# Performance work log

Hardware: AMD Instinct MI355X
Metric: run time of the kernel (lower is better)

Reference implementation:

```python
import jax, jax.numpy as jnp
import numpy as np

B, L, S, D, H = 2, 384, 384, 512, 256
BASE_TEMP = 10.0
LN_EPS = 1e-5


def setup_inputs() -> dict:
    key = jax.random.key(0)
    ks = jax.random.split(key, 12)
    return {
        "q": jax.random.normal(ks[0], (B, L, D), jnp.float32),
        "k": jax.random.normal(ks[1], (B, S, D), jnp.float32),
        "q_global": jax.random.normal(ks[2], (B, D), jnp.float32),
        "k_global": jax.random.normal(ks[3], (B, D), jnp.float32),
        "W1": jax.random.normal(ks[4], (4 * D, H), jnp.float32) * (1.0 / np.sqrt(4 * D)),
        "b1": jnp.zeros((H,), jnp.float32),
        "gamma": jnp.ones((H,), jnp.float32),
        "beta": jnp.zeros((H,), jnp.float32),
        "W2": jax.random.normal(ks[5], (H, 1), jnp.float32) * (1.0 / np.sqrt(H)),
        "b2": jnp.zeros((1,), jnp.float32),
        "gumbel_u": jax.random.uniform(ks[6], (B, L, S, 2), jnp.float32),
    }


def reference(q, k, q_global, k_global, W1, b1, gamma, beta, W2, b2, gumbel_u):
    d = q.shape[-1]
    # Decompose Linear(4D,H) on the [q, k, q_global, k_global] concat into
    # four per-tensor projections; sum broadcasts to the pairwise grid.
    Wq, Wk, Wqg, Wkg = jnp.split(W1, 4, axis=0)  # each [D,H]
    hq = q @ Wq + (q_global @ Wqg)[:, None, :]   # [B,L,H]
    hk = k @ Wk + (k_global @ Wkg)[:, None, :]   # [B,S,H]
    h = hq[:, :, None, :] + hk[:, None, :, :] + b1  # [B,L,S,H]
    h = jax.nn.gelu(h, approximate=False)
    mu = jnp.mean(h, axis=-1, keepdims=True)
    var = jnp.mean(jnp.square(h - mu), axis=-1, keepdims=True)
    h = (h - mu) * jax.lax.rsqrt(var + LN_EPS) * gamma + beta
    thresholds = (h @ W2)[..., 0] + b2[0]  # [B,L,S]
    sim = jnp.einsum("bld,bsd->bls", q, k) / jnp.sqrt(jnp.float32(d))
    logits = (sim - thresholds) / BASE_TEMP
    binary_logits = jnp.stack([-logits, logits], axis=-1)  # [B,L,S,2]
    u = jnp.clip(gumbel_u, 1e-6, 1.0 - 1e-6)
    g = -jnp.log(-jnp.log(u))
    soft = jax.nn.softmax(binary_logits + g, axis=-1)  # tau=1.0
    hard = jax.nn.one_hot(jnp.argmax(soft, axis=-1), 2, dtype=soft.dtype)
    y = hard + soft - jax.lax.stop_gradient(soft)  # straight-through
    return y[..., 1][:, None, :, :]  # [B,1,L,S]
```

## Files before the change

kernel.cpp:

```cpp
#include <hip/hip_runtime.h>
#include <hip/hip_bf16.h>
#include <math.h>

#define Bb 2
#define Lq 384
#define Sk 384
#define Dd 512
#define Hh 256

#define LIST_CAP 65536

#define HQD_OFF  0
#define HKD_OFF  (HQD_OFF + Bb*Lq*Hh*8)
#define GQD_OFF  (HKD_OFF + Bb*Sk*Hh*8)
#define GKD_OFF  (GQD_OFF + Bb*Hh*8)
#define HQ_OFF   (GKD_OFF + Bb*Hh*8)
#define HK_OFF   (HQ_OFF + Bb*Lq*Hh*4)
#define SIM0_OFF (HK_OFF + Bb*Sk*Hh*4)
#define SIM1_OFF (SIM0_OFF + Bb*Lq*Sk*4)
#define SCAL_OFF (SIM1_OFF + Bb*Lq*Sk*4)
#define GW_OFF   (SCAL_OFF + 64)
#define CNT_OFF  (GW_OFF + 1024)
#define LIST_OFF (CNT_OFF + 64)

__global__ __launch_bounds__(256) void smalls_kernel(
    const float* __restrict__ qg, const float* __restrict__ kg,
    const float* __restrict__ W1,
    const float* __restrict__ gam, const float* __restrict__ bet,
    const float* __restrict__ W2, const float* __restrict__ b2,
    double* __restrict__ gq_d, double* __restrict__ gk_d,
    float* __restrict__ gw_out, float* __restrict__ scal)
{
    __shared__ double red[64][5];
    __shared__ float2 red2[256];
    int bx  = blockIdx.x;
    int tid = threadIdx.x;
    if (bx < 16) {
        int isK = bx & 1;
        int b   = (bx >> 1) & 1;
        int hc  = bx >> 2;
        int hl  = tid >> 2;
        int dp  = tid & 3;
        int h   = hc * 64 + hl;
        const float* gv = (isK ? kg : qg) + b * Dd;
        const float* wp = W1 + (isK ? 3 : 2) * Dd * Hh + h;
        int d0 = dp * 128;
        double a0 = 0, a1 = 0, a2 = 0, a3 = 0;
        for (int i = 0; i < 128; i += 4) {
            int d = d0 + i;
            a0 = fma((double)gv[d + 0], (double)wp[(d + 0) * Hh], a0);
            a1 = fma((double)gv[d + 1], (double)wp[(d + 1) * Hh], a1);
            a2 = fma((double)gv[d + 2], (double)wp[(d + 2) * Hh], a2);
            a3 = fma((double)gv[d + 3], (double)wp[(d + 3) * Hh], a3);
        }
        red[hl][dp] = ((a0 + a1) + (a2 + a3));
        __syncthreads();
        if (dp == 0) {
            double s = (red[hl][0] + red[hl][1]) + (red[hl][2] + red[hl][3]);
            (isK ? gk_d : gq_d)[b * Hh + h] = s;
        }
    } else {
        float w2v = W2[tid];
        float gwv = gam[tid] * w2v;
        gw_out[tid] = gwv;
        red2[tid] = make_float2(gwv, bet[tid] * w2v);
        __syncthreads();
        for (int o = 128; o > 0; o >>= 1) {
            if (tid < o) {
                red2[tid].x += red2[tid + o].x;
                red2[tid].y += red2[tid + o].y;
            }
            __syncthreads();
        }
        if (tid == 0) {
            scal[0] = red2[0].x;
            scal[1] = red2[0].y + b2[0];
        }
    }
}

__global__ __launch_bounds__(512) void projd_kernel(
    const float* __restrict__ q, const float* __restrict__ k,
    const float* __restrict__ W1, const float* __restrict__ b1,
    const double* __restrict__ gq_d, const double* __restrict__ gk_d,
    double* __restrict__ hq_d, double* __restrict__ hk_d,
    float* __restrict__ hq, float* __restrict__ hk)
{
    __shared__ __align__(16) float smem[8 * 512];
    float  (*tile)[512] = (float (*)[512])smem;
    double (*pbuf)[256] = (double (*)[256])smem;
    int tid = threadIdx.x;
    int h   = tid & 255;
    int dh  = tid >> 8;
    int bx = blockIdx.x;
    bool isQ = bx < 96;
    int bb = isQ ? bx : bx - 96;
    int b  = bb / 48;
    int rg = bb % 48;
    const float*  src = isQ ? q : k;
    const double* gl  = isQ ? gq_d : gk_d;
    int woff = isQ ? 0 : Dd * Hh;
    double* dstd = isQ ? hq_d : hk_d;
    float*  dstf = isQ ? hq : hk;

    int base = (b * Lq + rg * 8) * Dd;
    for (int i = tid; i < 1024; i += 512)
        *reinterpret_cast<float4*>(&smem[i * 4]) =
            *reinterpret_cast<const float4*>(src + base + i * 4);
    __syncthreads();

    const float* wp = W1 + woff + (dh * 256) * Hh + h;
    int dbase = dh * 256;
    double acc[8];
#pragma unroll
    for (int r = 0; r < 8; ++r) acc[r] = 0.0;
#pragma unroll 2
    for (int d4 = 0; d4 < 256; d4 += 4) {
        double w0 = (double)wp[(d4 + 0) * Hh];
        double w1 = (double)wp[(d4 + 1) * Hh];
        double w2 = (double)wp[(d4 + 2) * Hh];
        double w3 = (double)wp[(d4 + 3) * Hh];
#pragma unroll
        for (int r = 0; r < 8; ++r) {
            float4 tv = *reinterpret_cast<const float4*>(&tile[r][dbase + d4]);
            acc[r] = fma((double)tv.x, w0, acc[r]);
            acc[r] = fma((double)tv.y, w1, acc[r]);
            acc[r] = fma((double)tv.z, w2, acc[r]);
            acc[r] = fma((double)tv.w, w3, acc[r]);
        }
    }
    __syncthreads();
    if (dh == 1) {
#pragma unroll
        for (int r = 0; r < 8; ++r) pbuf[r][h] = acc[r];
    }
    __syncthreads();
    if (dh == 0) {
        double gd  = gl[b * Hh + h];
        double b1d = isQ ? (double)b1[h] : 0.0;
        int ob = (b * Lq + rg * 8) * Hh + h;
#pragma unroll
        for (int r = 0; r < 8; ++r) {
            double tot = (acc[r] + pbuf[r][h]) + gd;
            dstd[ob + r * Hh] = tot;
            dstf[ob + r * Hh] = (float)(tot + b1d);
        }
    }
}

__global__ __launch_bounds__(256) void sim_kernel(
    const float* __restrict__ q, const float* __restrict__ k,
    float* __restrict__ sim01)
{
    __shared__ __align__(16) float qs[32][132];
    __shared__ __align__(16) float ks[32][132];
    int tid = threadIdx.x;
    int bx = blockIdx.x;
    int kc = (bx >= Bb * 144) ? 1 : 0;
    int r  = bx - kc * Bb * 144;
    int b  = r / 144;  r %= 144;
    int lt = r / 12, st = r % 12;
    int tl = tid >> 4, ts = tid & 15;
    const float* qb = q + (b * Lq + lt * 32) * Dd;
    const float* kb = k + (b * Sk + st * 32) * Dd;
    float a00 = 0.f, a01 = 0.f, a10 = 0.f, a11 = 0.f;
    for (int c = kc * 256; c < kc * 256 + 256; c += 128) {
        __syncthreads();
        for (int i = tid; i < 1024; i += 256) {
            int row = i >> 5;
            int c4  = (i & 31) << 2;
            *reinterpret_cast<float4*>(&qs[row][c4]) =
                *reinterpret_cast<const float4*>(qb + row * Dd + c + c4);
            *reinterpret_cast<float4*>(&ks[row][c4]) =
                *reinterpret_cast<const float4*>(kb + row * Dd + c + c4);
        }
        __syncthreads();
#pragma unroll 2
        for (int dd = 0; dd < 128; dd += 4) {
            float4 q0 = *reinterpret_cast<const float4*>(&qs[tl][dd]);
            float4 q1 = *reinterpret_cast<const float4*>(&qs[tl + 16][dd]);
            float4 k0 = *reinterpret_cast<const float4*>(&ks[ts][dd]);
            float4 k1 = *reinterpret_cast<const float4*>(&ks[ts + 16][dd]);
            a00 = fmaf(q0.x, k0.x, a00); a00 = fmaf(q0.y, k0.y, a00);
            a00 = fmaf(q0.z, k0.z, a00); a00 = fmaf(q0.w, k0.w, a00);
            a01 = fmaf(q0.x, k1.x, a01); a01 = fmaf(q0.y, k1.y, a01);
            a01 = fmaf(q0.z, k1.z, a01); a01 = fmaf(q0.w, k1.w, a01);
            a10 = fmaf(q1.x, k0.x, a10); a10 = fmaf(q1.y, k0.y, a10);
            a10 = fmaf(q1.z, k0.z, a10); a10 = fmaf(q1.w, k0.w, a10);
            a11 = fmaf(q1.x, k1.x, a11); a11 = fmaf(q1.y, k1.y, a11);
            a11 = fmaf(q1.z, k1.z, a11); a11 = fmaf(q1.w, k1.w, a11);
        }
    }
    const float sc = 0.04419417382415922f;
    float* dst = sim01 + kc * (Bb * Lq * Sk);
    int l0 = lt * 32 + tl, s0 = st * 32 + ts;
    dst[(b * Lq + l0)      * Sk + s0]      = a00 * sc;
    dst[(b * Lq + l0)      * Sk + s0 + 16] = a01 * sc;
    dst[(b * Lq + l0 + 16) * Sk + s0]      = a10 * sc;
    dst[(b * Lq + l0 + 16) * Sk + s0 + 16] = a11 * sc;
}

__device__ __forceinline__ void gelu2(float2 hqv, float2 hkv, float2 gwv,
                                      float2& s1, float2& s2, float2& sw)
{
    const float P2   = 0.23164189f;
    const float A1f = 0.254829592f, A2f = -0.284496736f, A3f = 1.421413741f,
                A4f = -1.453152027f, A5f = 1.061405429f;
    const float NL2EH = -0.72134752044448170f;

    float xa = hqv.x + hkv.x,        xb = hqv.y + hkv.y;
    float axa = fabsf(xa),           axb = fabsf(xb);
    float dda = fmaf(P2, axa, 1.0f), ddb = fmaf(P2, axb, 1.0f);
    float ta = __builtin_amdgcn_rcpf(dda), tb = __builtin_amdgcn_rcpf(ddb);
    float x2a = xa * xa,             x2b = xb * xb;
    float exa = __builtin_amdgcn_exp2f(x2a * NL2EH);
    float exb = __builtin_amdgcn_exp2f(x2b * NL2EH);
    float sa = fmaf(A5f, ta, A4f),   sb = fmaf(A5f, tb, A4f);
    sa = fmaf(sa, ta, A3f);          sb = fmaf(sb, tb, A3f);
    sa = fmaf(sa, ta, A2f);          sb = fmaf(sb, tb, A2f);
    sa = fmaf(sa, ta, A1f);          sb = fmaf(sb, tb, A1f);
    sa = sa * ta;                    sb = sb * tb;
    float Ea = fmaf(-sa, exa, 1.0f), Eb = fmaf(-sb, exb, 1.0f);
    float ya = fmaf(axa, Ea, xa),    yb = fmaf(axb, Eb, xb);
    s1.x += ya;                      s1.y += yb;
    s2.x = fmaf(ya, ya, s2.x);       s2.y = fmaf(yb, yb, s2.y);
    sw.x = fmaf(ya, gwv.x, sw.x);    sw.y = fmaf(yb, gwv.y, sw.y);
}

__global__ __launch_bounds__(256) void main_kernel(
    const float* __restrict__ hq, const float* __restrict__ hk,
    const float* __restrict__ sim0, const float* __restrict__ sim1,
    const float* __restrict__ gw_in, const float* __restrict__ scal,
    const float* __restrict__ gu, float* __restrict__ out,
    int* __restrict__ cnt, int* __restrict__ list)
{
    __shared__ __align__(16) float hq_t[16][260];
    __shared__ __align__(16) float hk_t[16][260];
    __shared__ __align__(16) float gw_s[256];
    int tid = threadIdx.x;
    int bx = blockIdx.x;
    int b  = bx / (24 * 24);
    int r  = bx % (24 * 24);
    int lt = r / 24, st = r % 24;

    const float* hqb = hq + (b * Lq + lt * 16) * Hh;
    const float* hkb = hk + (b * Sk + st * 16) * Hh;
#pragma unroll
    for (int i = 0; i < 4; ++i) {
        int idx4 = i * 256 + tid;
        int row  = idx4 >> 6;
        int col4 = (idx4 & 63) << 2;
        *reinterpret_cast<float4*>(&hq_t[row][col4]) =
            *reinterpret_cast<const float4*>(hqb + row * Hh + col4);
        *reinterpret_cast<float4*>(&hk_t[row][col4]) =
            *reinterpret_cast<const float4*>(hkb + row * Hh + col4);
    }
    gw_s[tid] = gw_in[tid];
    __syncthreads();
    float gwsum  = scal[0];
    float bconst = scal[1];

    int tl = tid >> 4, ts = tid & 15;
    float2 s1 = make_float2(0.f, 0.f);
    float2 s2 = make_float2(0.f, 0.f);
    float2 sw = make_float2(0.f, 0.f);
#pragma unroll 2
    for (int h4 = 0; h4 < Hh; h4 += 4) {
        float4 hq4 = *reinterpret_cast<const float4*>(&hq_t[tl][h4]);
        float4 hk4 = *reinterpret_cast<const float4*>(&hk_t[ts][h4]);
        float4 gw4 = *reinterpret_cast<const float4*>(&gw_s[h4]);
        gelu2(make_float2(hq4.x, hq4.y), make_float2(hk4.x, hk4.y),
              make_float2(gw4.x, gw4.y), s1, s2, sw);
        gelu2(make_float2(hq4.z, hq4.w), make_float2(hk4.z, hk4.w),
              make_float2(gw4.z, gw4.w), s1, s2, sw);
    }
    float S1 = s1.x + s1.y;
    float S2 = s2.x + s2.y;
    float SW = 0.5f * (sw.x + sw.y);
    float mu   = S1 * (1.0f / 512.0f);
    float var  = S2 * (1.0f / 1024.0f) - mu * mu;
    float rstd = rsqrtf(var + 1e-5f);
    float thr  = rstd * (SW - mu * gwsum) + bconst;

    int l = lt * 16 + tl, s = st * 16 + ts;
    int idx = (b * Lq + l) * Sk + s;
    float  sv = sim0[idx] + sim1[idx];
    float2 uv = reinterpret_cast<const float2*>(gu)[idx];
    float u0 = fminf(fmaxf(uv.x, 1e-6f), 1.0f - 1e-6f);
    float u1 = fminf(fmaxf(uv.y, 1e-6f), 1.0f - 1e-6f);
    float g0 = -logf(-logf(u0));
    float g1 = -logf(-logf(u1));
    float t  = 0.2f * (sv - thr) + (g1 - g0);
    out[idx] = t > 0.0f ? 1.0f : 0.0f;
    if (fabsf(t) < 1e-3f) {
        int p = atomicAdd(cnt, 1);
        if (p < LIST_CAP) list[p] = idx;
    }
}

__global__ __launch_bounds__(256) void cleanup_kernel(
    const float* __restrict__ q, const float* __restrict__ k,
    const double* __restrict__ hq_d, const double* __restrict__ hk_d,
    const float* __restrict__ b1,
    const float* __restrict__ gam, const float* __restrict__ bet,
    const float* __restrict__ W2, const float* __restrict__ b2,
    const float* __restrict__ gu, float* __restrict__ out,
    const int* __restrict__ cnt, const int* __restrict__ list)
{
    __shared__ double s0[256], s1[256], s2[256], s3[256];
    int tid = threadIdx.x;
    int n = *cnt;
    if (n > LIST_CAP) n = LIST_CAP;
    if (n == 0) return;

    double gw  = (double)gam[tid] * (double)W2[tid];
    double b1d = (double)b1[tid];
    s0[tid] = (double)bet[tid] * (double)W2[tid];
    s1[tid] = gw;
    __syncthreads();
    for (int o = 128; o > 0; o >>= 1) {
        if (tid < o) { s0[tid] += s0[tid + o]; s1[tid] += s1[tid + o]; }
        __syncthreads();
    }
    double bconst = s0[0] + (double)b2[0];
    double gwsum  = s1[0];
    __syncthreads();

    for (int it = blockIdx.x; it < n; it += gridDim.x) {
        int idx = list[it];
        int b   = idx / (Lq * Sk);
        int rem = idx % (Lq * Sk);
        int l = rem / Sk, s = rem % Sk;
        double x = (hq_d[(b * Lq + l) * Hh + tid]
                  + hk_d[(b * Sk + s) * Hh + tid]) + b1d;
        double y = 0.5 * x * (1.0 + erf(x * 0.70710678118654752440));
        const float* qrow = q + (b * Lq + l) * Dd;
        const float* krow = k + (b * Sk + s) * Dd;
        double sp = (double)qrow[tid] * (double)krow[tid]
                  + (double)qrow[tid + 256] * (double)krow[tid + 256];
        s0[tid] = y; s1[tid] = y * y; s2[tid] = y * gw; s3[tid] = sp;
        __syncthreads();
        for (int o = 128; o > 0; o >>= 1) {
            if (tid < o) {
                s0[tid] += s0[tid + o]; s1[tid] += s1[tid + o];
                s2[tid] += s2[tid + o]; s3[tid] += s3[tid + o];
            }
            __syncthreads();
        }
        if (tid == 0) {
            double mu   = s0[0] * (1.0 / 256.0);
            double var  = s1[0] * (1.0 / 256.0) - mu * mu;
            double rstd = 1.0 / sqrt(var + 1e-5);
            double thr  = rstd * (s2[0] - mu * gwsum) + bconst;
            double simv = s3[0] / 22.627416997969522;
            float2 uv = reinterpret_cast<const float2*>(gu)[idx];
            double u0 = fmin(fmax((double)uv.x, 1e-6), 1.0 - 1e-6);
            double u1 = fmin(fmax((double)uv.y, 1e-6), 1.0 - 1e-6);
            double g0 = -log(-log(u0));
            double g1 = -log(-log(u1));
            double t  = 0.2 * (simv - thr) + (g1 - g0);
            out[idx] = t > 0.0 ? 1.0f : 0.0f;
        }
        __syncthreads();
    }
}

extern "C" void kernel_launch(void* const* d_in, const int* in_sizes, int n_in,
                              void* d_out, int out_size, void* d_ws, size_t ws_size,
                              hipStream_t stream)
{
    const float* q   = (const float*)d_in[0];
    const float* k   = (const float*)d_in[1];
    const float* qg  = (const float*)d_in[2];
    const float* kg  = (const float*)d_in[3];
    const float* W1  = (const float*)d_in[4];
    const float* b1  = (const float*)d_in[5];
    const float* gam = (const float*)d_in[6];
    const float* bet = (const float*)d_in[7];
    const float* W2  = (const float*)d_in[8];
    const float* b2  = (const float*)d_in[9];
    const float* gu  = (const float*)d_in[10];
    float* out = (float*)d_out;

    char*   ws   = (char*)d_ws;
    double* hq_d = (double*)(ws + HQD_OFF);
    double* hk_d = (double*)(ws + HKD_OFF);
    double* gq_d = (double*)(ws + GQD_OFF);
    double* gk_d = (double*)(ws + GKD_OFF);
    float*  hq   = (float*)(ws + HQ_OFF);
    float*  hk   = (float*)(ws + HK_OFF);
    float*  sim0 = (float*)(ws + SIM0_OFF);
    float*  sim1 = (float*)(ws + SIM1_OFF);
    float*  scal = (float*)(ws + SCAL_OFF);
    float*  gw   = (float*)(ws + GW_OFF);
    int*    cnt  = (int*)(ws + CNT_OFF);
    int*    list = (int*)(ws + LIST_OFF);

    hipMemsetAsync(cnt, 0, sizeof(int), stream);
    smalls_kernel<<<17, 256, 0, stream>>>(
        qg, kg, W1, gam, bet, W2, b2, gq_d, gk_d, gw, scal);
    projd_kernel<<<192, 512, 0, stream>>>(
        q, k, W1, b1, gq_d, gk_d, hq_d, hk_d, hq, hk);
    sim_kernel<<<2 * Bb * 144, 256, 0, stream>>>(q, k, sim0);
    main_kernel<<<Bb * 24 * 24, 256, 0, stream>>>(
        hq, hk, sim0, sim1, gw, scal, gu, out, cnt, list);
    cleanup_kernel<<<768, 256, 0, stream>>>(
        q, k, hq_d, hk_d, b1, gam, bet, W2, b2, gu, out, cnt, list);
}
```

Measured before the change: 167.6 us.

## Fuse small precompute into projection kernel and double main kernel row tile

Removes the separate smalls kernel and the memset. The global-vector projections and the gamma·W2 scalars are now computed inside projd_kernel, with the counter reset done there too. main_kernel now gives each thread two L rows, so every hk element loaded from shared memory is reused twice. It also computes gw on the fly from gam and W2. This cuts two launches and some memory traffic, but each projd block now redoes the global projection, and main_kernel launches half as many blocks with more registers per thread.

```diff
diff --git a/kernel.cpp b/kernel.cpp
--- a/kernel.cpp
+++ b/kernel.cpp
@@ -12,83 +12,30 @@
 
 #define HQD_OFF  0
 #define HKD_OFF  (HQD_OFF + Bb*Lq*Hh*8)
-#define GQD_OFF  (HKD_OFF + Bb*Sk*Hh*8)
-#define GKD_OFF  (GQD_OFF + Bb*Hh*8)
-#define HQ_OFF   (GKD_OFF + Bb*Hh*8)
+#define HQ_OFF   (HKD_OFF + Bb*Sk*Hh*8)
 #define HK_OFF   (HQ_OFF + Bb*Lq*Hh*4)
 #define SIM0_OFF (HK_OFF + Bb*Sk*Hh*4)
 #define SIM1_OFF (SIM0_OFF + Bb*Lq*Sk*4)
 #define SCAL_OFF (SIM1_OFF + Bb*Lq*Sk*4)
-#define GW_OFF   (SCAL_OFF + 64)
-#define CNT_OFF  (GW_OFF + 1024)
+#define CNT_OFF  (SCAL_OFF + 64)
 #define LIST_OFF (CNT_OFF + 64)
 
-__global__ __launch_bounds__(256) void smalls_kernel(
+__global__ __launch_bounds__(512) void projd_kernel(
+    const float* __restrict__ q, const float* __restrict__ k,
     const float* __restrict__ qg, const float* __restrict__ kg,
-    const float* __restrict__ W1,
+    const float* __restrict__ W1, const float* __restrict__ b1,
     const float* __restrict__ gam, const float* __restrict__ bet,
     const float* __restrict__ W2, const float* __restrict__ b2,
-    double* __restrict__ gq_d, double* __restrict__ gk_d,
-    float* __restrict__ gw_out, float* __restrict__ scal)
-{
-    __shared__ double red[64][5];
-    __shared__ float2 red2[256];
-    int bx  = blockIdx.x;
-    int tid = threadIdx.x;
-    if (bx < 16) {
-        int isK = bx & 1;
-        int b   = (bx >> 1) & 1;
-        int hc  = bx >> 2;
-        int hl  = tid >> 2;
-        int dp  = tid & 3;
-        int h   = hc * 64 + hl;
-        const float* gv = (isK ? kg : qg) + b * Dd;
-        const float* wp = W1 + (isK ? 3 : 2) * Dd * Hh + h;
-        int d0 = dp * 128;
-        double a0 = 0, a1 = 0, a2 = 0, a3 = 0;
-        for (int i = 0; i < 128; i += 4) {
-            int d = d0 + i;
-            a0 = fma((double)gv[d + 0], (double)wp[(d + 0) * Hh], a0);
-            a1 = fma((double)gv[d + 1], (double)wp[(d + 1) * Hh], a1);
-            a2 = fma((double)gv[d + 2], (double)wp[(d + 2) * Hh], a2);
-            a3 = fma((double)gv[d + 3], (double)wp[(d + 3) * Hh], a3);
-        }
-        red[hl][dp] = ((a0 + a1) + (a2 + a3));
-        __syncthreads();
-        if (dp == 0) {
-            double s = (red[hl][0] + red[hl][1]) + (red[hl][2] + red[hl][3]);
-            (isK ? gk_d : gq_d)[b * Hh + h] = s;
-        }
-    } else {
-        float w2v = W2[tid];
-        float gwv = gam[tid] * w2v;
-        gw_out[tid] = gwv;
-        red2[tid] = make_float2(gwv, bet[tid] * w2v);
-        __syncthreads();
-        for (int o = 128; o > 0; o >>= 1) {
-            if (tid < o) {
-                red2[tid].x += red2[tid + o].x;
-                red2[tid].y += red2[tid + o].y;
-            }
-            __syncthreads();
-        }
-        if (tid == 0) {
-            scal[0] = red2[0].x;
-            scal[1] = red2[0].y + b2[0];
-        }
-    }
-}
-
-__global__ __launch_bounds__(512) void projd_kernel(
-    const float* __restrict__ q, const float* __restrict__ k,
-    const float* __restrict__ W1, const float* __restrict__ b1,
-    const double* __restrict__ gq_d, const double* __restrict__ gk_d,
     double* __restrict__ hq_d, double* __restrict__ hk_d,
-    float* __restrict__ hq, float* __restrict__ hk)
-{
-    __shared__ __align__(16) float smem[8 * 512];
-    float  (*tile)[512] = (float (*)[512])smem;
-    double (*pbuf)[256] = (double (*)[256])smem;
+    float* __restrict__ hq, float* __restrict__ hk,
+    float* __restrict__ scal, int* __restrict__ cnt)
+{
+    __shared__ __align__(16) double sbuf[9 * 256];
+    float  (*tile)[512] = (float (*)[512])sbuf;
+    float*  gvd  = (float*)(sbuf + 2048);
+    double (*pbuf)[256] = (double (*)[256])sbuf;
+    double* gbuf = sbuf + 2048;
+
     int tid = threadIdx.x;
     int h   = tid & 255;
     int dh  = tid >> 8;
@@ -97,29 +44,55 @@
     int bb = isQ ? bx : bx - 96;
     int b  = bb / 48;
     int rg = bb % 48;
-    const float*  src = isQ ? q : k;
-    const double* gl  = isQ ? gq_d : gk_d;
-    int woff = isQ ? 0 : Dd * Hh;
+    const float* src = isQ ? q : k;
+    const float* gl  = isQ ? qg : kg;
+    int woff  = isQ ? 0 : Dd * Hh;
+    int woffg = isQ ? 2 * Dd * Hh : 3 * Dd * Hh;
     double* dstd = isQ ? hq_d : hk_d;
     float*  dstf = isQ ? hq : hk;
 
+    if (bx == 0 && tid == 0) *cnt = 0;
+    if (bx == 0 && tid < 64) {
+        float a = 0.f, c = 0.f;
+        for (int i = tid; i < 256; i += 64) {
+            float w2v = W2[i];
+            a = fmaf(gam[i], w2v, a);
+            c = fmaf(bet[i], w2v, c);
+        }
+        for (int o = 32; o > 0; o >>= 1) {
+            a += __shfl_xor(a, o, 64);
+            c += __shfl_xor(c, o, 64);
+        }
+        if (tid == 0) { scal[0] = a; scal[1] = c + b2[0]; }
+    }
+
     int base = (b * Lq + rg * 8) * Dd;
     for (int i = tid; i < 1024; i += 512)
-        *reinterpret_cast<float4*>(&smem[i * 4]) =
+        *reinterpret_cast<float4*>((float*)tile + i * 4) =
             *reinterpret_cast<const float4*>(src + base + i * 4);
-    __syncthreads();
-
-    const float* wp = W1 + woff + (dh * 256) * Hh + h;
+    if (tid < 128)
+        *reinterpret_cast<float4*>(gvd + tid * 4) =
+            *reinterpret_cast<const float4*>(gl + b * Dd + tid * 4);
+    __syncthreads();
+
+    const float* wp = W1 + woff  + (dh * 256) * Hh + h;
+    const float* gp = W1 + woffg + (dh * 256) * Hh + h;
     int dbase = dh * 256;
     double acc[8];
 #pragma unroll
     for (int r = 0; r < 8; ++r) acc[r] = 0.0;
+    double gacc = 0.0;
 #pragma unroll 2
     for (int d4 = 0; d4 < 256; d4 += 4) {
         double w0 = (double)wp[(d4 + 0) * Hh];
         double w1 = (double)wp[(d4 + 1) * Hh];
         double w2 = (double)wp[(d4 + 2) * Hh];
         double w3 = (double)wp[(d4 + 3) * Hh];
+        float4 gv = *reinterpret_cast<const float4*>(&gvd[dbase + d4]);
+        gacc = fma((double)gv.x, (double)gp[(d4 + 0) * Hh], gacc);
+        gacc = fma((double)gv.y, (double)gp[(d4 + 1) * Hh], gacc);
+        gacc = fma((double)gv.z, (double)gp[(d4 + 2) * Hh], gacc);
+        gacc = fma((double)gv.w, (double)gp[(d4 + 3) * Hh], gacc);
 #pragma unroll
         for (int r = 0; r < 8; ++r) {
             float4 tv = *reinterpret_cast<const float4*>(&tile[r][dbase + d4]);
@@ -133,10 +106,11 @@
     if (dh == 1) {
 #pragma unroll
         for (int r = 0; r < 8; ++r) pbuf[r][h] = acc[r];
+        gbuf[h] = gacc;
     }
     __syncthreads();
     if (dh == 0) {
-        double gd  = gl[b * Hh + h];
+        double gd  = gacc + gbuf[h];
         double b1d = isQ ? (double)b1[h] : 0.0;
         int ob = (b * Lq + rg * 8) * Hh + h;
 #pragma unroll
@@ -230,71 +204,86 @@
 __global__ __launch_bounds__(256) void main_kernel(
     const float* __restrict__ hq, const float* __restrict__ hk,
     const float* __restrict__ sim0, const float* __restrict__ sim1,
-    const float* __restrict__ gw_in, const float* __restrict__ scal,
+    const float* __restrict__ gam, const float* __restrict__ W2,
+    const float* __restrict__ scal,
     const float* __restrict__ gu, float* __restrict__ out,
     int* __restrict__ cnt, int* __restrict__ list)
 {
-    __shared__ __align__(16) float hq_t[16][260];
+    __shared__ __align__(16) float hq_t[32][260];
     __shared__ __align__(16) float hk_t[16][260];
     __shared__ __align__(16) float gw_s[256];
     int tid = threadIdx.x;
     int bx = blockIdx.x;
-    int b  = bx / (24 * 24);
-    int r  = bx % (24 * 24);
+    int b  = bx / (12 * 24);
+    int r  = bx % (12 * 24);
     int lt = r / 24, st = r % 24;
 
-    const float* hqb = hq + (b * Lq + lt * 16) * Hh;
+    const float* hqb = hq + (b * Lq + lt * 32) * Hh;
     const float* hkb = hk + (b * Sk + st * 16) * Hh;
 #pragma unroll
-    for (int i = 0; i < 4; ++i) {
+    for (int i = 0; i < 8; ++i) {
         int idx4 = i * 256 + tid;
         int row  = idx4 >> 6;
         int col4 = (idx4 & 63) << 2;
         *reinterpret_cast<float4*>(&hq_t[row][col4]) =
             *reinterpret_cast<const float4*>(hqb + row * Hh + col4);
+    }
+#pragma unroll
+    for (int i = 0; i < 4; ++i) {
+        int idx4 = i * 256 + tid;
+        int row  = idx4 >> 6;
+        int col4 = (idx4 & 63) << 2;
         *reinterpret_cast<float4*>(&hk_t[row][col4]) =
             *reinterpret_cast<const float4*>(hkb + row * Hh + col4);
     }
-    gw_s[tid] = gw_in[tid];
+    gw_s[tid] = gam[tid] * W2[tid];
     __syncthreads();
     float gwsum  = scal[0];
     float bconst = scal[1];
 
     int tl = tid >> 4, ts = tid & 15;
-    float2 s1 = make_float2(0.f, 0.f);
-    float2 s2 = make_float2(0.f, 0.f);
-    float2 sw = make_float2(0.f, 0.f);
+    float2 s1a = make_float2(0.f, 0.f), s2a = s1a, swa = s1a;
+    float2 s1b = s1a, s2b = s1a, swb = s1a;
 #pragma unroll 2
     for (int h4 = 0; h4 < Hh; h4 += 4) {
-        float4 hq4 = *reinterpret_cast<const float4*>(&hq_t[tl][h4]);
-        float4 hk4 = *reinterpret_cast<const float4*>(&hk_t[ts][h4]);
-        float4 gw4 = *reinterpret_cast<const float4*>(&gw_s[h4]);
-        gelu2(make_float2(hq4.x, hq4.y), make_float2(hk4.x, hk4.y),
-              make_float2(gw4.x, gw4.y), s1, s2, sw);
-        gelu2(make_float2(hq4.z, hq4.w), make_float2(hk4.z, hk4.w),
-              make_float2(gw4.z, gw4.w), s1, s2, sw);
-    }
-    float S1 = s1.x + s1.y;
-    float S2 = s2.x + s2.y;
-    float SW = 0.5f * (sw.x + sw.y);
-    float mu   = S1 * (1.0f / 512.0f);
-    float var  = S2 * (1.0f / 1024.0f) - mu * mu;
-    float rstd = rsqrtf(var + 1e-5f);
-    float thr  = rstd * (SW - mu * gwsum) + bconst;
-
-    int l = lt * 16 + tl, s = st * 16 + ts;
-    int idx = (b * Lq + l) * Sk + s;
-    float  sv = sim0[idx] + sim1[idx];
-    float2 uv = reinterpret_cast<const float2*>(gu)[idx];
-    float u0 = fminf(fmaxf(uv.x, 1e-6f), 1.0f - 1e-6f);
-    float u1 = fminf(fmaxf(uv.y, 1e-6f), 1.0f - 1e-6f);
-    float g0 = -logf(-logf(u0));
-    float g1 = -logf(-logf(u1));
-    float t  = 0.2f * (sv - thr) + (g1 - g0);
-    out[idx] = t > 0.0f ? 1.0f : 0.0f;
-    if (fabsf(t) < 1e-3f) {
-        int p = atomicAdd(cnt, 1);
-        if (p < LIST_CAP) list[p] = idx;
+        float4 ha = *reinterpret_cast<const float4*>(&hq_t[tl][h4]);
+        float4 hb = *reinterpret_cast<const float4*>(&hq_t[tl + 16][h4]);
+        float4 kk = *reinterpret_cast<const float4*>(&hk_t[ts][h4]);
+        float4 g4 = *reinterpret_cast<const float4*>(&gw_s[h4]);
+        gelu2(make_float2(ha.x, ha.y), make_float2(kk.x, kk.y),
+              make_float2(g4.x, g4.y), s1a, s2a, swa);
+        gelu2(make_float2(ha.z, ha.w), make_float2(kk.z, kk.w),
+              make_float2(g4.z, g4.w), s1a, s2a, swa);
+        gelu2(make_float2(hb.x, hb.y), make_float2(kk.x, kk.y),
+              make_float2(g4.x, g4.y), s1b, s2b, swb);
+        gelu2(make_float2(hb.z, hb.w), make_float2(kk.z, kk.w),
+              make_float2(g4.z, g4.w), s1b, s2b, swb);
+    }
+
+#pragma unroll
+    for (int e = 0; e < 2; ++e) {
+        float S1 = e ? (s1b.x + s1b.y) : (s1a.x + s1a.y);
+        float S2 = e ? (s2b.x + s2b.y) : (s2a.x + s2a.y);
+        float SW = 0.5f * (e ? (swb.x + swb.y) : (swa.x + swa.y));
+        float mu   = S1 * (1.0f / 512.0f);
+        float var  = S2 * (1.0f / 1024.0f) - mu * mu;
+        float rstd = rsqrtf(var + 1e-5f);
+        float thr  = rstd * (SW - mu * gwsum) + bconst;
+
+        int l = lt * 32 + tl + e * 16, s = st * 16 + ts;
+        int idx = (b * Lq + l) * Sk + s;
+        float  sv = sim0[idx] + sim1[idx];
+        float2 uv = reinterpret_cast<const float2*>(gu)[idx];
+        float u0 = fminf(fmaxf(uv.x, 1e-6f), 1.0f - 1e-6f);
+        float u1 = fminf(fmaxf(uv.y, 1e-6f), 1.0f - 1e-6f);
+        float g0 = -logf(-logf(u0));
+        float g1 = -logf(-logf(u1));
+        float t  = 0.2f * (sv - thr) + (g1 - g0);
+        out[idx] = t > 0.0f ? 1.0f : 0.0f;
+        if (fabsf(t) < 1e-3f) {
+            int p = atomicAdd(cnt, 1);
+            if (p < LIST_CAP) list[p] = idx;
+        }
     }
 }
 
@@ -385,25 +374,20 @@
     char*   ws   = (char*)d_ws;
     double* hq_d = (double*)(ws + HQD_OFF);
     double* hk_d = (double*)(ws + HKD_OFF);
-    double* gq_d = (double*)(ws + GQD_OFF);
-    double* gk_d = (double*)(ws + GKD_OFF);
     float*  hq   = (float*)(ws + HQ_OFF);
     float*  hk   = (float*)(ws + HK_OFF);
     float*  sim0 = (float*)(ws + SIM0_OFF);
     float*  sim1 = (float*)(ws + SIM1_OFF);
     float*  scal = (float*)(ws + SCAL_OFF);
-    float*  gw   = (float*)(ws + GW_OFF);
     int*    cnt  = (int*)(ws + CNT_OFF);
     int*    list = (int*)(ws + LIST_OFF);
 
-    hipMemsetAsync(cnt, 0, sizeof(int), stream);
-    smalls_kernel<<<17, 256, 0, stream>>>(
-        qg, kg, W1, gam, bet, W2, b2, gq_d, gk_d, gw, scal);
     projd_kernel<<<192, 512, 0, stream>>>(
-        q, k, W1, b1, gq_d, gk_d, hq_d, hk_d, hq, hk);
+        q, k, qg, kg, W1, b1, gam, bet, W2, b2,
+        hq_d, hk_d, hq, hk, scal, cnt);
     sim_kernel<<<2 * Bb * 144, 256, 0, stream>>>(q, k, sim0);
-    main_kernel<<<Bb * 24 * 24, 256, 0, stream>>>(
-        hq, hk, sim0, sim1, gw, scal, gu, out, cnt, list);
+    main_kernel<<<Bb * 12 * 24, 256, 0, stream>>>(
+        hq, hk, sim0, sim1, gam, W2, scal, gu, out, cnt, list);
     cleanup_kernel<<<768, 256, 0, stream>>>(
         q, k, hq_d, hk_d, b1, gam, bet, W2, b2, gu, out, cnt, list);
 }
```

Result: slower. 175.1 us (+4.5%).

## Split fp64 projection over D into partials, enlarge main tile to 32 rows

Applied to the files above, without the earlier changes.

The fp64 projection kernel is now split along D into four partial blocks per four-row group (1536 blocks instead of 192), with a separate finalize kernel that reduces the partials and adds the global terms. This is meant to fix the poor occupancy of the fp64 GEMV. The main kernel now handles 32 query rows per block, so each thread computes two outputs and the hk tile is reused across them. The hipMemsetAsync of the counter is folded into smalls_kernel, and gamma*W2 is computed inline. The cost is an extra launch, extra partial-buffer traffic, and half as many main-kernel blocks.

```diff
diff --git a/kernel.cpp b/kernel.cpp
--- a/kernel.cpp
+++ b/kernel.cpp
@@ -9,18 +9,19 @@
 #define Hh 256
 
 #define LIST_CAP 65536
+#define NROWS (2 * Bb * Lq)
 
 #define HQD_OFF  0
 #define HKD_OFF  (HQD_OFF + Bb*Lq*Hh*8)
-#define GQD_OFF  (HKD_OFF + Bb*Sk*Hh*8)
+#define PART_OFF (HKD_OFF + Bb*Sk*Hh*8)
+#define GQD_OFF  (PART_OFF + NROWS*4*Hh*8)
 #define GKD_OFF  (GQD_OFF + Bb*Hh*8)
 #define HQ_OFF   (GKD_OFF + Bb*Hh*8)
 #define HK_OFF   (HQ_OFF + Bb*Lq*Hh*4)
 #define SIM0_OFF (HK_OFF + Bb*Sk*Hh*4)
 #define SIM1_OFF (SIM0_OFF + Bb*Lq*Sk*4)
 #define SCAL_OFF (SIM1_OFF + Bb*Lq*Sk*4)
-#define GW_OFF   (SCAL_OFF + 64)
-#define CNT_OFF  (GW_OFF + 1024)
+#define CNT_OFF  (SCAL_OFF + 64)
 #define LIST_OFF (CNT_OFF + 64)
 
 __global__ __launch_bounds__(256) void smalls_kernel(
@@ -29,7 +30,7 @@
     const float* __restrict__ gam, const float* __restrict__ bet,
     const float* __restrict__ W2, const float* __restrict__ b2,
     double* __restrict__ gq_d, double* __restrict__ gk_d,
-    float* __restrict__ gw_out, float* __restrict__ scal)
+    float* __restrict__ scal, int* __restrict__ cnt)
 {
     __shared__ double red[64][5];
     __shared__ float2 red2[256];
@@ -60,10 +61,9 @@
             (isK ? gk_d : gq_d)[b * Hh + h] = s;
         }
     } else {
+        if (tid == 0) *cnt = 0;
         float w2v = W2[tid];
-        float gwv = gam[tid] * w2v;
-        gw_out[tid] = gwv;
-        red2[tid] = make_float2(gwv, bet[tid] * w2v);
+        red2[tid] = make_float2(gam[tid] * w2v, bet[tid] * w2v);
         __syncthreads();
         for (int o = 128; o > 0; o >>= 1) {
             if (tid < o) {
@@ -79,71 +79,90 @@
     }
 }
 
-__global__ __launch_bounds__(512) void projd_kernel(
+__global__ __launch_bounds__(256) void projd_part_kernel(
     const float* __restrict__ q, const float* __restrict__ k,
-    const float* __restrict__ W1, const float* __restrict__ b1,
-    const double* __restrict__ gq_d, const double* __restrict__ gk_d,
-    double* __restrict__ hq_d, double* __restrict__ hk_d,
-    float* __restrict__ hq, float* __restrict__ hk)
-{
-    __shared__ __align__(16) float smem[8 * 512];
-    float  (*tile)[512] = (float (*)[512])smem;
-    double (*pbuf)[256] = (double (*)[256])smem;
-    int tid = threadIdx.x;
-    int h   = tid & 255;
-    int dh  = tid >> 8;
-    int bx = blockIdx.x;
-    bool isQ = bx < 96;
-    int bb = isQ ? bx : bx - 96;
-    int b  = bb / 48;
-    int rg = bb % 48;
-    const float*  src = isQ ? q : k;
-    const double* gl  = isQ ? gq_d : gk_d;
+    const float* __restrict__ W1, double* __restrict__ part)
+{
+    __shared__ __align__(16) float tile[4][128];
+    int tid = threadIdx.x;
+    int bx  = blockIdx.x;
+    int ds  = bx & 3;
+    int rgid = bx >> 2;
+    bool isQ = rgid < 192;
+    int bb = isQ ? rgid : rgid - 192;
+    int b  = bb / 96;
+    int rg = bb % 96;
+    const float* src = isQ ? q : k;
     int woff = isQ ? 0 : Dd * Hh;
-    double* dstd = isQ ? hq_d : hk_d;
-    float*  dstf = isQ ? hq : hk;
-
-    int base = (b * Lq + rg * 8) * Dd;
-    for (int i = tid; i < 1024; i += 512)
-        *reinterpret_cast<float4*>(&smem[i * 4]) =
-            *reinterpret_cast<const float4*>(src + base + i * 4);
+    int rowbase = b * Lq + rg * 4;
+
+    if (tid < 128) {
+        int row = tid >> 5;
+        int c4  = (tid & 31) << 2;
+        *reinterpret_cast<float4*>(&tile[row][c4]) =
+            *reinterpret_cast<const float4*>(
+                src + (size_t)(rowbase + row) * Dd + ds * 128 + c4);
+    }
     __syncthreads();
 
-    const float* wp = W1 + woff + (dh * 256) * Hh + h;
-    int dbase = dh * 256;
-    double acc[8];
-#pragma unroll
-    for (int r = 0; r < 8; ++r) acc[r] = 0.0;
+    const float* wp = W1 + woff + (ds * 128) * Hh + tid;
+    double a0 = 0.0, a1 = 0.0, a2 = 0.0, a3 = 0.0;
 #pragma unroll 2
-    for (int d4 = 0; d4 < 256; d4 += 4) {
+    for (int d4 = 0; d4 < 128; d4 += 4) {
         double w0 = (double)wp[(d4 + 0) * Hh];
         double w1 = (double)wp[(d4 + 1) * Hh];
         double w2 = (double)wp[(d4 + 2) * Hh];
         double w3 = (double)wp[(d4 + 3) * Hh];
+        float4 t0 = *reinterpret_cast<const float4*>(&tile[0][d4]);
+        float4 t1 = *reinterpret_cast<const float4*>(&tile[1][d4]);
+        float4 t2 = *reinterpret_cast<const float4*>(&tile[2][d4]);
+        float4 t3 = *reinterpret_cast<const float4*>(&tile[3][d4]);
+        a0 = fma((double)t0.x, w0, a0); a0 = fma((double)t0.y, w1, a0);
+        a0 = fma((double)t0.z, w2, a0); a0 = fma((double)t0.w, w3, a0);
+        a1 = fma((double)t1.x, w0, a1); a1 = fma((double)t1.y, w1, a1);
+        a1 = fma((double)t1.z, w2, a1); a1 = fma((double)t1.w, w3, a1);
+        a2 = fma((double)t2.x, w0, a2); a2 = fma((double)t2.y, w1, a2);
+        a2 = fma((double)t2.z, w2, a2); a2 = fma((double)t2.w, w3, a2);
+        a3 = fma((double)t3.x, w0, a3); a3 = fma((double)t3.y, w1, a3);
+        a3 = fma((double)t3.z, w2, a3); a3 = fma((double)t3.w, w3, a3);
+    }
+    int rowglob = (isQ ? 0 : Bb * Lq) + rowbase;
+    size_t obase = ((size_t)rowglob * 4 + ds) * Hh + tid;
+    part[obase]            = a0;
+    part[obase + 4 * Hh]   = a1;
+    part[obase + 8 * Hh]   = a2;
+    part[obase + 12 * Hh]  = a3;
+}
+
+__global__ __launch_bounds__(256) void finalize_kernel(
+    const double* __restrict__ part,
+    const double* __restrict__ gq_d, const double* __restrict__ gk_d,
+    const float* __restrict__ b1,
+    double* __restrict__ hq_d, double* __restrict__ hk_d,
+    float* __restrict__ hq, float* __restrict__ hk)
+{
+    int tid = threadIdx.x;
+    int bx  = blockIdx.x;
 #pragma unroll
-        for (int r = 0; r < 8; ++r) {
-            float4 tv = *reinterpret_cast<const float4*>(&tile[r][dbase + d4]);
-            acc[r] = fma((double)tv.x, w0, acc[r]);
-            acc[r] = fma((double)tv.y, w1, acc[r]);
-            acc[r] = fma((double)tv.z, w2, acc[r]);
-            acc[r] = fma((double)tv.w, w3, acc[r]);
-        }
-    }
-    __syncthreads();
-    if (dh == 1) {
-#pragma unroll
-        for (int r = 0; r < 8; ++r) pbuf[r][h] = acc[r];
-    }
-    __syncthreads();
-    if (dh == 0) {
-        double gd  = gl[b * Hh + h];
-        double b1d = isQ ? (double)b1[h] : 0.0;
-        int ob = (b * Lq + rg * 8) * Hh + h;
-#pragma unroll
-        for (int r = 0; r < 8; ++r) {
-            double tot = (acc[r] + pbuf[r][h]) + gd;
-            dstd[ob + r * Hh] = tot;
-            dstf[ob + r * Hh] = (float)(tot + b1d);
+    for (int r = 0; r < 2; ++r) {
+        int rowglob = bx * 2 + r;
+        bool isQ = rowglob < Bb * Lq;
+        int rr = isQ ? rowglob : rowglob - Bb * Lq;
+        int b  = rr / Lq;
+        size_t pbase = ((size_t)rowglob * 4) * Hh + tid;
+        double p0 = part[pbase];
+        double p1 = part[pbase + 1 * Hh];
+        double p2 = part[pbase + 2 * Hh];
+        double p3 = part[pbase + 3 * Hh];
+        double gl = (isQ ? gq_d : gk_d)[b * Hh + tid];
+        double tot = ((p0 + p1) + (p2 + p3)) + gl;
+        size_t o = (size_t)rr * Hh + tid;
+        if (isQ) {
+            hq_d[o] = tot;
+            hq[o]   = (float)(tot + (double)b1[tid]);
+        } else {
+            hk_d[o] = tot;
+            hk[o]   = (float)tot;
         }
     }
 }
@@ -230,71 +249,86 @@
 __global__ __launch_bounds__(256) void main_kernel(
     const float* __restrict__ hq, const float* __restrict__ hk,
     const float* __restrict__ sim0, const float* __restrict__ sim1,
-    const float* __restrict__ gw_in, const float* __restrict__ scal,
+    const float* __restrict__ gam, const float* __restrict__ W2,
+    const float* __restrict__ scal,
     const float* __restrict__ gu, float* __restrict__ out,
     int* __restrict__ cnt, int* __restrict__ list)
 {
-    __shared__ __align__(16) float hq_t[16][260];
+    __shared__ __align__(16) float hq_t[32][260];
     __shared__ __align__(16) float hk_t[16][260];
     __shared__ __align__(16) float gw_s[256];
     int tid = threadIdx.x;
     int bx = blockIdx.x;
-    int b  = bx / (24 * 24);
-    int r  = bx % (24 * 24);
+    int b  = bx / (12 * 24);
+    int r  = bx % (12 * 24);
     int lt = r / 24, st = r % 24;
 
-    const float* hqb = hq + (b * Lq + lt * 16) * Hh;
+    const float* hqb = hq + (b * Lq + lt * 32) * Hh;
     const float* hkb = hk + (b * Sk + st * 16) * Hh;
+#pragma unroll
+    for (int i = 0; i < 8; ++i) {
+        int idx4 = i * 256 + tid;
+        int row  = idx4 >> 6;
+        int col4 = (idx4 & 63) << 2;
+        *reinterpret_cast<float4*>(&hq_t[row][col4]) =
+            *reinterpret_cast<const float4*>(hqb + row * Hh + col4);
+    }
 #pragma unroll
     for (int i = 0; i < 4; ++i) {
         int idx4 = i * 256 + tid;
         int row  = idx4 >> 6;
         int col4 = (idx4 & 63) << 2;
-        *reinterpret_cast<float4*>(&hq_t[row][col4]) =
-            *reinterpret_cast<const float4*>(hqb + row * Hh + col4);
         *reinterpret_cast<float4*>(&hk_t[row][col4]) =
             *reinterpret_cast<const float4*>(hkb + row * Hh + col4);
     }
-    gw_s[tid] = gw_in[tid];
+    gw_s[tid] = gam[tid] * W2[tid];
     __syncthreads();
     float gwsum  = scal[0];
     float bconst = scal[1];
 
     int tl = tid >> 4, ts = tid & 15;
-    float2 s1 = make_float2(0.f, 0.f);
-    float2 s2 = make_float2(0.f, 0.f);
-    float2 sw = make_float2(0.f, 0.f);
+    float2 s1a = make_float2(0.f, 0.f), s2a = s1a, swa = s1a;
+    float2 s1b = s1a, s2b = s1a, swb = s1a;
 #pragma unroll 2
     for (int h4 = 0; h4 < Hh; h4 += 4) {
-        float4 hq4 = *reinterpret_cast<const float4*>(&hq_t[tl][h4]);
-        float4 hk4 = *reinterpret_cast<const float4*>(&hk_t[ts][h4]);
-        float4 gw4 = *reinterpret_cast<const float4*>(&gw_s[h4]);
-        gelu2(make_float2(hq4.x, hq4.y), make_float2(hk4.x, hk4.y),
-              make_float2(gw4.x, gw4.y), s1, s2, sw);
-        gelu2(make_float2(hq4.z, hq4.w), make_float2(hk4.z, hk4.w),
-              make_float2(gw4.z, gw4.w), s1, s2, sw);
-    }
-    float S1 = s1.x + s1.y;
-    float S2 = s2.x + s2.y;
-    float SW = 0.5f * (sw.x + sw.y);
-    float mu   = S1 * (1.0f / 512.0f);
-    float var  = S2 * (1.0f / 1024.0f) - mu * mu;
-    float rstd = rsqrtf(var + 1e-5f);
-    float thr  = rstd * (SW - mu * gwsum) + bconst;
-
-    int l = lt * 16 + tl, s = st * 16 + ts;
-    int idx = (b * Lq + l) * Sk + s;
-    float  sv = sim0[idx] + sim1[idx];
-    float2 uv = reinterpret_cast<const float2*>(gu)[idx];
-    float u0 = fminf(fmaxf(uv.x, 1e-6f), 1.0f - 1e-6f);
-    float u1 = fminf(fmaxf(uv.y, 1e-6f), 1.0f - 1e-6f);
-    float g0 = -logf(-logf(u0));
-    float g1 = -logf(-logf(u1));
-    float t  = 0.2f * (sv - thr) + (g1 - g0);
-    out[idx] = t > 0.0f ? 1.0f : 0.0f;
-    if (fabsf(t) < 1e-3f) {
-        int p = atomicAdd(cnt, 1);
-        if (p < LIST_CAP) list[p] = idx;
+        float4 ha = *reinterpret_cast<const float4*>(&hq_t[tl][h4]);
+        float4 hb = *reinterpret_cast<const float4*>(&hq_t[tl + 16][h4]);
+        float4 kk = *reinterpret_cast<const float4*>(&hk_t[ts][h4]);
+        float4 g4 = *reinterpret_cast<const float4*>(&gw_s[h4]);
+        gelu2(make_float2(ha.x, ha.y), make_float2(kk.x, kk.y),
+              make_float2(g4.x, g4.y), s1a, s2a, swa);
+        gelu2(make_float2(ha.z, ha.w), make_float2(kk.z, kk.w),
+              make_float2(g4.z, g4.w), s1a, s2a, swa);
+        gelu2(make_float2(hb.x, hb.y), make_float2(kk.x, kk.y),
+              make_float2(g4.x, g4.y), s1b, s2b, swb);
+        gelu2(make_float2(hb.z, hb.w), make_float2(kk.z, kk.w),
+              make_float2(g4.z, g4.w), s1b, s2b, swb);
+    }
+
+#pragma unroll
+    for (int e = 0; e < 2; ++e) {
+        float S1 = e ? (s1b.x + s1b.y) : (s1a.x + s1a.y);
+        float S2 = e ? (s2b.x + s2b.y) : (s2a.x + s2a.y);
+        float SW = 0.5f * (e ? (swb.x + swb.y) : (swa.x + swa.y));
+        float mu   = S1 * (1.0f / 512.0f);
+        float var  = S2 * (1.0f / 1024.0f) - mu * mu;
+        float rstd = rsqrtf(var + 1e-5f);
+        float thr  = rstd * (SW - mu * gwsum) + bconst;
+
+        int l = lt * 32 + tl + e * 16, s = st * 16 + ts;
+        int idx = (b * Lq + l) * Sk + s;
+        float  sv = sim0[idx] + sim1[idx];
+        float2 uv = reinterpret_cast<const float2*>(gu)[idx];
+        float u0 = fminf(fmaxf(uv.x, 1e-6f), 1.0f - 1e-6f);
+        float u1 = fminf(fmaxf(uv.y, 1e-6f), 1.0f - 1e-6f);
+        float g0 = -logf(-logf(u0));
+        float g1 = -logf(-logf(u1));
+        float t  = 0.2f * (sv - thr) + (g1 - g0);
+        out[idx] = t > 0.0f ? 1.0f : 0.0f;
+        if (fabsf(t) < 1e-3f) {
+            int p = atomicAdd(cnt, 1);
+            if (p < LIST_CAP) list[p] = idx;
+        }
     }
 }
 
@@ -385,6 +419,7 @@
     char*   ws   = (char*)d_ws;
     double* hq_d = (double*)(ws + HQD_OFF);
     double* hk_d = (double*)(ws + HKD_OFF);
+    double* part = (double*)(ws + PART_OFF);
     double* gq_d = (double*)(ws + GQD_OFF);
     double* gk_d = (double*)(ws + GKD_OFF);
     float*  hq   = (float*)(ws + HQ_OFF);
@@ -392,18 +427,17 @@
     float*  sim0 = (float*)(ws + SIM0_OFF);
     float*  sim1 = (float*)(ws + SIM1_OFF);
     float*  scal = (float*)(ws + SCAL_OFF);
-    float*  gw   = (float*)(ws + GW_OFF);
     int*    cnt  = (int*)(ws + CNT_OFF);
     int*    list = (int*)(ws + LIST_OFF);
 
-    hipMemsetAsync(cnt, 0, sizeof(int), stream);
     smalls_kernel<<<17, 256, 0, stream>>>(
-        qg, kg, W1, gam, bet, W2, b2, gq_d, gk_d, gw, scal);
-    projd_kernel<<<192, 512, 0, stream>>>(
-        q, k, W1, b1, gq_d, gk_d, hq_d, hk_d, hq, hk);
+        qg, kg, W1, gam, bet, W2, b2, gq_d, gk_d, scal, cnt);
+    projd_part_kernel<<<NROWS, 256, 0, stream>>>(q, k, W1, part);
+    finalize_kernel<<<NROWS / 2, 256, 0, stream>>>(
+        part, gq_d, gk_d, b1, hq_d, hk_d, hq, hk);
     sim_kernel<<<2 * Bb * 144, 256, 0, stream>>>(q, k, sim0);
-    main_kernel<<<Bb * 24 * 24, 256, 0, stream>>>(
-        hq, hk, sim0, sim1, gw, scal, gu, out, cnt, list);
+    main_kernel<<<Bb * 12 * 24, 256, 0, stream>>>(
+        hq, hk, sim0, sim1, gam, W2, scal, gu, out, cnt, list);
     cleanup_kernel<<<768, 256, 0, stream>>>(
         q, k, hq_d, hk_d, b1, gam, bet, W2, b2, gu, out, cnt, list);
 }
```

Result: slower. 171.1 us (+2.1%).
